# Kernel tuning notes

Measured on AMD Instinct MI355X. Metric: run time of the kernel, lower is better.

The kernel has to match this reference:

```python
import jax, jax.numpy as jnp
import numpy as np
import math

B, N, F_IN, F_OUT = 16, 2048, 256, 64


def setup_inputs() -> dict:
    key = jax.random.key(0)
    k1, k2, k3, k4 = jax.random.split(key, 4)
    x = jax.random.normal(k1, (B, N, F_IN), dtype=jnp.float32)
    adj = jax.random.randint(k2, (B, N, N), 0, 2, dtype=jnp.int32)
    stdv = 1.0 / math.sqrt(F_OUT)
    weight = jax.random.uniform(k3, (F_IN, F_OUT), dtype=jnp.float32, minval=-stdv, maxval=stdv)
    # weight2 stdv = 1/sqrt(1) = 1.0
    weight2 = jax.random.uniform(k4, (2 * F_OUT, 1), dtype=jnp.float32, minval=-1.0, maxval=1.0)
    return {"x": x, "adj": adj, "weight": weight, "weight2": weight2}


def reference(x, adj, weight, weight2):
    # h[b,n,o] = (x @ weight)  -- shared linear projection
    h = jnp.einsum("bni,io->bno", x, weight)
    Fo = weight.shape[1]
    # Split additive-attention vector: e_ij = relu(h_i . a_src + h_j . a_dst)
    # Mathematically identical to cat([h_i, h_j]) @ weight2 of the original.
    a_src = weight2[:Fo, 0]
    a_dst = weight2[Fo:, 0]
    s_src = jnp.einsum("bno,o->bn", h, a_src)  # [B, N]
    s_dst = jnp.einsum("bno,o->bn", h, a_dst)  # [B, N]
    e = jax.nn.relu(s_src[:, :, None] + s_dst[:, None, :])  # [B, N, N]
    NEG = jnp.float32(-9e15)
    scores = jnp.where(adj > 0, e, NEG)
    attention = jax.nn.softmax(scores, axis=2)  # softmax over neighbors j
    # dropout = 0.0 / eval mode -> identity
    out = jnp.einsum("bij,bjo->bio", attention, h)  # [B, N, F_OUT]
    return out
```

## Files before the change

kernel.cpp:

```cpp
#include <hip/hip_runtime.h>
#include <hip/hip_bf16.h>

#define BB 16
#define NN 2048
#define FIN 256
#define FO 64

typedef __bf16 bf16x8 __attribute__((ext_vector_type(8)));
typedef float  f32x4  __attribute__((ext_vector_type(4)));
typedef int    i32x4  __attribute__((ext_vector_type(4)));

__global__ void k0_prep(const float* __restrict__ weight, const float* __restrict__ w2,
                        __bf16* __restrict__ Wt, float* __restrict__ vsrc,
                        float* __restrict__ vdst) {
    int t = threadIdx.x;
    for (int idx = t; idx < FIN * FO; idx += 256) {
        int k = idx >> 6, o = idx & 63;
        Wt[o * FIN + k] = (__bf16)weight[idx];
    }
    float a = 0.f, d = 0.f;
    for (int o = 0; o < FO; ++o) {
        float wv = weight[t * FO + o];
        a += wv * w2[o];
        d += wv * w2[FO + o];
    }
    vsrc[t] = a;
    vdst[t] = d;
}

__global__ __launch_bounds__(256) void k1_gemm(
    const float* __restrict__ x, const __bf16* __restrict__ Wt,
    const float* __restrict__ vsrc, const float* __restrict__ vdst,
    __bf16* __restrict__ hT, float* __restrict__ s_src, float* __restrict__ s_dst) {
    int lane = threadIdx.x & 63, w = threadIdx.x >> 6;
    int quad = lane >> 4, m = lane & 15;
    int Rbase = blockIdx.x * 64 + w * 16;
    int R = Rbase + m;
    const float* xr = x + (long)R * FIN;

    f32x4 acc[4] = {};
    float ps = 0.f, pd = 0.f;

#pragma unroll
    for (int k0 = 0; k0 < FIN; k0 += 32) {
        int kb = k0 + quad * 8;
        float4 x0 = *(const float4*)(xr + kb);
        float4 x1 = *(const float4*)(xr + kb + 4);
        float4 u0 = *(const float4*)(vsrc + kb);
        float4 u1 = *(const float4*)(vsrc + kb + 4);
        float4 t0 = *(const float4*)(vdst + kb);
        float4 t1 = *(const float4*)(vdst + kb + 4);
        ps += x0.x * u0.x + x0.y * u0.y + x0.z * u0.z + x0.w * u0.w +
              x1.x * u1.x + x1.y * u1.y + x1.z * u1.z + x1.w * u1.w;
        pd += x0.x * t0.x + x0.y * t0.y + x0.z * t0.z + x0.w * t0.w +
              x1.x * t1.x + x1.y * t1.y + x1.z * t1.z + x1.w * t1.w;
        bf16x8 bf = {(__bf16)x0.x, (__bf16)x0.y, (__bf16)x0.z, (__bf16)x0.w,
                     (__bf16)x1.x, (__bf16)x1.y, (__bf16)x1.z, (__bf16)x1.w};
#pragma unroll
        for (int ot = 0; ot < 4; ++ot) {
            bf16x8 af = *(const bf16x8*)(Wt + (ot * 16 + m) * FIN + kb);
            acc[ot] = __builtin_amdgcn_mfma_f32_16x16x32_bf16(af, bf, acc[ot], 0, 0, 0);
        }
    }
    ps += __shfl_xor(ps, 16);
    ps += __shfl_xor(ps, 32);
    pd += __shfl_xor(pd, 16);
    pd += __shfl_xor(pd, 32);
    if (quad == 0) {
        s_src[R] = ps;
        s_dst[R] = pd;
    }
    int b = R >> 11;
    int nb = Rbase & (NN - 1);
#pragma unroll
    for (int ot = 0; ot < 4; ++ot) {
#pragma unroll
        for (int r = 0; r < 4; ++r) {
            int o = ot * 16 + quad * 4 + r;
            hT[((long)b * FO + o) * NN + nb + m] = (__bf16)acc[ot][r];
        }
    }
}

__global__ __launch_bounds__(256) void k2_attn(
    const int* __restrict__ adj, const float* __restrict__ s_src,
    const float* __restrict__ s_dst, const __bf16* __restrict__ hT,
    float* __restrict__ out) {
    int b = blockIdx.x >> 5;
    int i0 = (blockIdx.x & 31) << 6;
    int lane = threadIdx.x & 63, w = threadIdx.x >> 6;
    int quad = lane >> 4, m = lane & 15;
    int row = i0 + w * 16 + m;

    const float* sd = s_dst + b * NN;
    float mx = -3.0e38f;
    for (int j = lane; j < NN; j += 64) mx = fmaxf(mx, sd[j]);
#pragma unroll
    for (int off = 32; off >= 1; off >>= 1) mx = fmaxf(mx, __shfl_xor(mx, off));

    float ssrc = s_src[b * NN + row];
    float M = fmaxf(ssrc + mx, 0.f);

    const int* adjrow = adj + ((long)b * NN + row) * NN;
    const __bf16* hTb = hT + (long)b * FO * NN;

    f32x4 acc[4] = {};
    float lp = 0.f;

#pragma unroll 2
    for (int j0 = 0; j0 < NN; j0 += 32) {
        int jb = j0 + quad * 8;
        i32x4 a0 = __builtin_nontemporal_load((const i32x4*)(adjrow + jb));
        i32x4 a1 = __builtin_nontemporal_load((const i32x4*)(adjrow + jb) + 1);
        float4 d0 = *(const float4*)(sd + jb);
        float4 d1 = *(const float4*)(sd + jb + 4);

        float p0 = (a0.x > 0) ? __expf(fmaxf(ssrc + d0.x, 0.f) - M) : 0.f;
        float p1 = (a0.y > 0) ? __expf(fmaxf(ssrc + d0.y, 0.f) - M) : 0.f;
        float p2 = (a0.z > 0) ? __expf(fmaxf(ssrc + d0.z, 0.f) - M) : 0.f;
        float p3 = (a0.w > 0) ? __expf(fmaxf(ssrc + d0.w, 0.f) - M) : 0.f;
        float p4 = (a1.x > 0) ? __expf(fmaxf(ssrc + d1.x, 0.f) - M) : 0.f;
        float p5 = (a1.y > 0) ? __expf(fmaxf(ssrc + d1.y, 0.f) - M) : 0.f;
        float p6 = (a1.z > 0) ? __expf(fmaxf(ssrc + d1.z, 0.f) - M) : 0.f;
        float p7 = (a1.w > 0) ? __expf(fmaxf(ssrc + d1.w, 0.f) - M) : 0.f;
        lp += ((p0 + p1) + (p2 + p3)) + ((p4 + p5) + (p6 + p7));

        bf16x8 af = {(__bf16)p0, (__bf16)p1, (__bf16)p2, (__bf16)p3,
                     (__bf16)p4, (__bf16)p5, (__bf16)p6, (__bf16)p7};
        const __bf16* hb = hTb + jb;
#pragma unroll
        for (int ot = 0; ot < 4; ++ot) {
            bf16x8 bf = *(const bf16x8*)(hb + (ot * 16 + m) * NN);
            acc[ot] = __builtin_amdgcn_mfma_f32_16x16x32_bf16(af, bf, acc[ot], 0, 0, 0);
        }
    }

    lp += __shfl_xor(lp, 16);
    lp += __shfl_xor(lp, 32);

    float* outp = out + ((long)b * NN + i0 + w * 16) * FO;
#pragma unroll
    for (int r = 0; r < 4; ++r) {
        int orow = quad * 4 + r;
        float lr = __shfl(lp, orow);
        float inv = 1.0f / lr;
#pragma unroll
        for (int ot = 0; ot < 4; ++ot) {
            outp[(long)orow * FO + ot * 16 + m] = acc[ot][r] * inv;
        }
    }
}

extern "C" void kernel_launch(void* const* d_in, const int* in_sizes, int n_in,
                              void* d_out, int out_size, void* d_ws, size_t ws_size,
                              hipStream_t stream) {
    const float* x      = (const float*)d_in[0];
    const int*   adj    = (const int*)d_in[1];
    const float* weight = (const float*)d_in[2];
    const float* w2     = (const float*)d_in[3];
    float* out = (float*)d_out;

    char* ws = (char*)d_ws;
    __bf16* hT   = (__bf16*)ws;
    float* s_src = (float*)(ws + 4194304);
    float* s_dst = (float*)(ws + 4194304 + 131072);
    float* vsrc  = (float*)(ws + 4194304 + 262144);
    float* vdst  = (float*)(ws + 4194304 + 262144 + 1024);
    __bf16* Wt   = (__bf16*)(ws + 4194304 + 262144 + 2048);

    k0_prep<<<1, 256, 0, stream>>>(weight, w2, Wt, vsrc, vdst);
    k1_gemm<<<512, 256, 0, stream>>>(x, Wt, vsrc, vdst, hT, s_src, s_dst);
    k2_attn<<<512, 256, 0, stream>>>(adj, s_src, s_dst, hT, out);
}
```

Baseline: 475.3 us.

## Coalesce adjacency reads per row and stage probabilities through LDS

Rewrites the attention kernel so each wave reads whole contiguous adjacency row chunks with all 64 lanes, instead of each lane streaming 32 bytes from a different row. The computed probabilities go as bf16 into a per-wave shared buffer laid out to match the MFMA A-fragment, then are read back for the matrix multiply. The row-sum is now taken from the bf16-rounded values. This targets the dominant 256MB adj stream, which had poorly coalesced access, at the cost of extra LDS traffic, 64KB of shared memory per block (which limits occupancy), and a possible write bank-conflict pattern.

```diff
diff --git a/kernel.cpp b/kernel.cpp
--- a/kernel.cpp
+++ b/kernel.cpp
@@ -5,8 +5,10 @@
 #define NN 2048
 #define FIN 256
 #define FO 64
+#define CH 512
 
 typedef __bf16 bf16x8 __attribute__((ext_vector_type(8)));
+typedef __bf16 bf16x4 __attribute__((ext_vector_type(4)));
 typedef float  f32x4  __attribute__((ext_vector_type(4)));
 typedef int    i32x4  __attribute__((ext_vector_type(4)));
 
@@ -86,11 +88,12 @@
     const int* __restrict__ adj, const float* __restrict__ s_src,
     const float* __restrict__ s_dst, const __bf16* __restrict__ hT,
     float* __restrict__ out) {
+    __shared__ __bf16 pbuf[4][16 * CH];
     int b = blockIdx.x >> 5;
     int i0 = (blockIdx.x & 31) << 6;
     int lane = threadIdx.x & 63, w = threadIdx.x >> 6;
     int quad = lane >> 4, m = lane & 15;
-    int row = i0 + w * 16 + m;
+    int rowbase = i0 + w * 16;
 
     const float* sd = s_dst + b * NN;
     float mx = -3.0e38f;
@@ -98,47 +101,56 @@
 #pragma unroll
     for (int off = 32; off >= 1; off >>= 1) mx = fmaxf(mx, __shfl_xor(mx, off));
 
-    float ssrc = s_src[b * NN + row];
-    float M = fmaxf(ssrc + mx, 0.f);
-
-    const int* adjrow = adj + ((long)b * NN + row) * NN;
+    const float* ssp = s_src + b * NN + rowbase;
+    const int* adjb = adj + ((long)b * NN + rowbase) * NN;
     const __bf16* hTb = hT + (long)b * FO * NN;
+    __bf16* pb = pbuf[w];
 
     f32x4 acc[4] = {};
     float lp = 0.f;
 
-#pragma unroll 2
-    for (int j0 = 0; j0 < NN; j0 += 32) {
-        int jb = j0 + quad * 8;
-        i32x4 a0 = __builtin_nontemporal_load((const i32x4*)(adjrow + jb));
-        i32x4 a1 = __builtin_nontemporal_load((const i32x4*)(adjrow + jb) + 1);
-        float4 d0 = *(const float4*)(sd + jb);
-        float4 d1 = *(const float4*)(sd + jb + 4);
-
-        float p0 = (a0.x > 0) ? __expf(fmaxf(ssrc + d0.x, 0.f) - M) : 0.f;
-        float p1 = (a0.y > 0) ? __expf(fmaxf(ssrc + d0.y, 0.f) - M) : 0.f;
-        float p2 = (a0.z > 0) ? __expf(fmaxf(ssrc + d0.z, 0.f) - M) : 0.f;
-        float p3 = (a0.w > 0) ? __expf(fmaxf(ssrc + d0.w, 0.f) - M) : 0.f;
-        float p4 = (a1.x > 0) ? __expf(fmaxf(ssrc + d1.x, 0.f) - M) : 0.f;
-        float p5 = (a1.y > 0) ? __expf(fmaxf(ssrc + d1.y, 0.f) - M) : 0.f;
-        float p6 = (a1.z > 0) ? __expf(fmaxf(ssrc + d1.z, 0.f) - M) : 0.f;
-        float p7 = (a1.w > 0) ? __expf(fmaxf(ssrc + d1.w, 0.f) - M) : 0.f;
-        lp += ((p0 + p1) + (p2 + p3)) + ((p4 + p5) + (p6 + p7));
-
-        bf16x8 af = {(__bf16)p0, (__bf16)p1, (__bf16)p2, (__bf16)p3,
-                     (__bf16)p4, (__bf16)p5, (__bf16)p6, (__bf16)p7};
-        const __bf16* hb = hTb + jb;
+    for (int jc = 0; jc < NN; jc += CH) {
+        float4 sv0 = *(const float4*)(sd + jc + 4 * lane);
+        float4 sv1 = *(const float4*)(sd + jc + 256 + 4 * lane);
 #pragma unroll
-        for (int ot = 0; ot < 4; ++ot) {
-            bf16x8 bf = *(const bf16x8*)(hb + (ot * 16 + m) * NN);
-            acc[ot] = __builtin_amdgcn_mfma_f32_16x16x32_bf16(af, bf, acc[ot], 0, 0, 0);
+        for (int r = 0; r < 16; ++r) {
+            float sr = ssp[r];
+            float M = fmaxf(sr + mx, 0.f);
+            const int* ap = adjb + (long)r * NN + jc;
+            i32x4 a0 = __builtin_nontemporal_load((const i32x4*)ap + lane);
+            i32x4 a1 = __builtin_nontemporal_load((const i32x4*)(ap + 256) + lane);
+            float p0 = (a0.x > 0) ? __expf(fmaxf(sr + sv0.x, 0.f) - M) : 0.f;
+            float p1 = (a0.y > 0) ? __expf(fmaxf(sr + sv0.y, 0.f) - M) : 0.f;
+            float p2 = (a0.z > 0) ? __expf(fmaxf(sr + sv0.z, 0.f) - M) : 0.f;
+            float p3 = (a0.w > 0) ? __expf(fmaxf(sr + sv0.w, 0.f) - M) : 0.f;
+            float p4 = (a1.x > 0) ? __expf(fmaxf(sr + sv1.x, 0.f) - M) : 0.f;
+            float p5 = (a1.y > 0) ? __expf(fmaxf(sr + sv1.y, 0.f) - M) : 0.f;
+            float p6 = (a1.z > 0) ? __expf(fmaxf(sr + sv1.z, 0.f) - M) : 0.f;
+            float p7 = (a1.w > 0) ? __expf(fmaxf(sr + sv1.w, 0.f) - M) : 0.f;
+            bf16x4 k0v = {(__bf16)p0, (__bf16)p1, (__bf16)p2, (__bf16)p3};
+            bf16x4 k1v = {(__bf16)p4, (__bf16)p5, (__bf16)p6, (__bf16)p7};
+            int g0 = lane >> 3, u = (lane & 7) * 4;
+            *(bf16x4*)(pb + g0 * 512 + r * 32 + u) = k0v;
+            *(bf16x4*)(pb + (8 + g0) * 512 + r * 32 + u) = k1v;
+        }
+#pragma unroll
+        for (int ks = 0; ks < CH / 32; ++ks) {
+            bf16x8 af = *(const bf16x8*)(pb + (ks * 16 + m) * 32 + quad * 8);
+#pragma unroll
+            for (int e = 0; e < 8; ++e) lp += (float)af[e];
+            const __bf16* hb = hTb + jc + ks * 32 + quad * 8;
+#pragma unroll
+            for (int ot = 0; ot < 4; ++ot) {
+                bf16x8 bf = *(const bf16x8*)(hb + (ot * 16 + m) * NN);
+                acc[ot] = __builtin_amdgcn_mfma_f32_16x16x32_bf16(af, bf, acc[ot], 0, 0, 0);
+            }
         }
     }
 
     lp += __shfl_xor(lp, 16);
     lp += __shfl_xor(lp, 32);
 
-    float* outp = out + ((long)b * NN + i0 + w * 16) * FO;
+    float* outp = out + ((long)b * NN + rowbase) * FO;
 #pragma unroll
     for (int r = 0; r < 4; ++r) {
         int orow = quad * 4 + r;
```

After: 478.4 us. About the same (+0.6%).
